# Kernel optimization log

Measured on AMD Instinct MI355X. Metric: run time of the kernel, lower is better.

The kernel has to match this reference:

```python
import jax, jax.numpy as jnp
import numpy as np
from jax import lax


def _conv2d(x, w, b):
    # Plain VALID conv, NCHW / OIHW, stride 1 (matches nn.Conv2d(kernel_size=3))
    y = lax.conv_general_dilated(x, w, (1, 1), 'VALID',
                                 dimension_numbers=('NCHW', 'OIHW', 'NCHW'))
    return y + b.reshape(1, -1, 1, 1)


def _deform_conv2d(x, w, b, offset, mask):
    # Faithful torchvision.ops.DeformConv2d: stride 1, pad 0, dilation 1, groups 1.
    # offset: [B, 2*K, Ho, Wo] with (dy, dx) interleaved per kernel tap.
    B, C, H, W = x.shape
    Cout, _, KH, KW = w.shape
    K = KH * KW
    Ho, Wo = H - KH + 1, W - KW + 1
    off = offset.reshape(B, K, 2, Ho, Wo)
    ky, kx = jnp.meshgrid(jnp.arange(KH), jnp.arange(KW), indexing='ij')  # [KH,KW]
    ky = ky.reshape(1, K, 1, 1).astype(off.dtype)
    kx = kx.reshape(1, K, 1, 1).astype(off.dtype)
    # sampling positions p = p0 + p_k + offset
    py = off[:, :, 0] + ky + jnp.arange(Ho, dtype=off.dtype).reshape(1, 1, Ho, 1)  # [B,K,Ho,Wo]
    px = off[:, :, 1] + kx + jnp.arange(Wo, dtype=off.dtype).reshape(1, 1, 1, Wo)
    y0 = jnp.floor(py)
    x0 = jnp.floor(px)
    fy = py - y0
    fx = px - x0
    y0i = y0.astype(jnp.int32)
    x0i = x0.astype(jnp.int32)
    x_flat = x.reshape(B, C, H * W)

    def corner(yi, xi, wgt):
        # zero-padding outside image: invalid taps contribute 0
        valid = (yi >= 0) & (yi < H) & (xi >= 0) & (xi < W)
        idx = jnp.clip(yi, 0, H - 1) * W + jnp.clip(xi, 0, W - 1)  # [B,K,Ho,Wo]
        vals = jax.vmap(lambda xf, i: jnp.take(xf, i, axis=-1))(x_flat, idx)  # [B,C,K,Ho,Wo]
        return vals * (wgt * valid)[:, None]

    acc = corner(y0i, x0i, (1 - fy) * (1 - fx))
    acc = acc + corner(y0i, x0i + 1, (1 - fy) * fx)
    acc = acc + corner(y0i + 1, x0i, fy * (1 - fx))
    acc = acc + corner(y0i + 1, x0i + 1, fy * fx)
    if mask is not None:
        acc = acc * mask.reshape(B, 1, K, Ho, Wo)
    out = jnp.einsum('bckhw,ock->bohw', acc, w.reshape(Cout, C, K))
    return out + b.reshape(1, -1, 1, 1)


def setup_inputs() -> dict:
    key = jax.random.key(0)
    ks = jax.random.split(key, 9)
    B, Cin, H, W = 16, 12, 256, 256
    s = 0.05  # small init so learned offsets stay a few pixels
    return {
        'x':  jax.random.normal(ks[0], (B, Cin, H, W), jnp.float32),
        'w0': jax.random.normal(ks[1], (18, Cin, 3, 3), jnp.float32) * s,
        'b0': jax.random.normal(ks[2], (18,), jnp.float32) * s,
        'w1': jax.random.normal(ks[3], (16, Cin, 3, 3), jnp.float32) * s,
        'b1': jax.random.normal(ks[4], (16,), jnp.float32) * s,
        'w2': jax.random.normal(ks[5], (9, Cin, 3, 3), jnp.float32) * s,
        'b2': jax.random.normal(ks[6], (9,), jnp.float32) * s,
        'w3': jax.random.normal(ks[7], (16, Cin, 3, 3), jnp.float32) * s,
        'b3': jax.random.normal(ks[8], (16,), jnp.float32) * s,
    }


def reference(x, w0, b0, w1, b1, w2, b2, w3, b3):
    offset = _conv2d(x, w0, b0)                       # [B,18,254,254]
    x1 = _deform_conv2d(x, w1, b1, offset, None)      # [B,16,254,254]
    mask = jax.nn.sigmoid(_conv2d(x, w2, b2))         # [B,9,254,254]
    x2 = _deform_conv2d(x, w3, b3, offset, mask)      # [B,16,254,254]
    return (x1, x2)
```

## Files before the change

kernel.cpp:

```cpp
#include <hip/hip_runtime.h>
#include <math.h>

#define BATCH 16
#define CIN   12
#define HH    256
#define WW    256
#define KK    9
#define HO    254
#define WO    254
#define PIX   (HO*WO)
#define COUT  16
#define CHW   (HH*WW)

__device__ __forceinline__ int iclamp(int v, int lo, int hi) {
    return v < lo ? lo : (v > hi ? hi : v);
}

__global__ __launch_bounds__(256, 4) void dcn_f32(
    const float* __restrict__ x,
    const float* __restrict__ w0, const float* __restrict__ b0,
    const float* __restrict__ w1, const float* __restrict__ b1,
    const float* __restrict__ w2, const float* __restrict__ b2,
    const float* __restrict__ w3, const float* __restrict__ b3,
    float* __restrict__ out)
{
    __shared__ float wc[KK*CIN*28];
    __shared__ float ew[KK*CIN*32];

    const int tid = threadIdx.y*16 + threadIdx.x;

    for (int i = tid; i < KK*CIN*28; i += 256) {
        int k = i / (CIN*28);
        int r = i % (CIN*28);
        int c = r / 28;
        int o = r % 28;
        float v = 0.f;
        if (o < 18)      v = w0[(o*CIN + c)*KK + k];
        else if (o < 27) v = w2[((o-18)*CIN + c)*KK + k];
        wc[i] = v;
    }
    for (int i = tid; i < KK*CIN*32; i += 256) {
        int kc = i >> 5;
        int j  = i & 31;
        int k  = kc / CIN;
        int c  = kc % CIN;
        ew[i] = (j < 16) ? w1[(j*CIN + c)*KK + k]
                         : w3[((j-16)*CIN + c)*KK + k];
    }
    __syncthreads();

    const int b  = blockIdx.z;
    const int ho = blockIdx.y*16 + threadIdx.y;
    const int wo = blockIdx.x*16 + threadIdx.x;
    if (ho >= HO || wo >= WO) return;

    const float* xb = x + (size_t)b*CIN*CHW;

    float off[28];
    #pragma unroll
    for (int o = 0; o < 18; ++o) off[o] = b0[o];
    #pragma unroll
    for (int o = 0; o < 9;  ++o) off[18+o] = b2[o];
    off[27] = 0.f;

    #pragma unroll
    for (int k = 0; k < 9; ++k) {
        const int ky = k / 3, kx = k % 3;
        const float* xt = xb + (size_t)(ho+ky)*WW + (wo+kx);
        float xv[CIN];
        #pragma unroll
        for (int c = 0; c < CIN; ++c) xv[c] = xt[(size_t)c*CHW];
        #pragma unroll
        for (int c = 0; c < CIN; ++c) {
            const float v = xv[c];
            const float4* wrow = (const float4*)&wc[(k*CIN + c)*28];
            #pragma unroll
            for (int q = 0; q < 7; ++q) {
                float4 w4 = wrow[q];
                off[4*q+0] += w4.x * v;
                off[4*q+1] += w4.y * v;
                off[4*q+2] += w4.z * v;
                off[4*q+3] += w4.w * v;
            }
        }
    }

    float m[9];
    #pragma unroll
    for (int j = 0; j < 9; ++j) m[j] = 1.f / (1.f + expf(-off[18+j]));

    float acc1[16], acc2[16];
    #pragma unroll
    for (int o = 0; o < 16; ++o) { acc1[o] = b1[o]; acc2[o] = b3[o]; }

    #pragma unroll
    for (int k = 0; k < 9; ++k) {
        const float py = off[2*k]   + (float)(k/3) + (float)ho;
        const float px = off[2*k+1] + (float)(k%3) + (float)wo;
        const float y0f = floorf(py), x0f = floorf(px);
        const float fy = py - y0f, fx = px - x0f;
        const int y0 = (int)y0f, x0i = (int)x0f;
        const int y1 = y0 + 1,  x1i = x0i + 1;

        float w00 = (1.f-fy)*(1.f-fx);
        float w01 = (1.f-fy)*fx;
        float w10 = fy*(1.f-fx);
        float w11 = fy*fx;

        const bool vy0 = (unsigned)y0  < HH;
        const bool vy1 = (unsigned)y1  < HH;
        const bool vx0 = (unsigned)x0i < WW;
        const bool vx1 = (unsigned)x1i < WW;
        if (!(vy0 && vx0)) w00 = 0.f;
        if (!(vy0 && vx1)) w01 = 0.f;
        if (!(vy1 && vx0)) w10 = 0.f;
        if (!(vy1 && vx1)) w11 = 0.f;

        const int cy0 = iclamp(y0, 0, HH-1);
        const int cy1 = iclamp(y1, 0, HH-1);
        const int cx0 = iclamp(x0i, 0, WW-1);
        const int cx1 = iclamp(x1i, 0, WW-1);
        const int i00 = cy0*WW + cx0;
        const int i01 = cy0*WW + cx1;
        const int i10 = cy1*WW + cx0;
        const int i11 = cy1*WW + cx1;

        const float mk = m[k];

        #pragma unroll
        for (int h = 0; h < 2; ++h) {
            float g00[6], g01[6], g10[6], g11[6];
            #pragma unroll
            for (int j = 0; j < 6; ++j) {
                const float* xc = xb + (size_t)(6*h + j)*CHW;
                g00[j] = xc[i00];
                g01[j] = xc[i01];
                g10[j] = xc[i10];
                g11[j] = xc[i11];
            }
            #pragma unroll
            for (int j = 0; j < 6; ++j) {
                const int c = 6*h + j;
                const float v  = w00*g00[j] + w01*g01[j] + w10*g10[j] + w11*g11[j];
                const float vm = v * mk;
                const float4* wr = (const float4*)&ew[(k*CIN + c)*32];
                #pragma unroll
                for (int q = 0; q < 4; ++q) {
                    float4 a  = wr[q];
                    float4 bb = wr[q+4];
                    acc1[4*q+0] += a.x  * v;
                    acc1[4*q+1] += a.y  * v;
                    acc1[4*q+2] += a.z  * v;
                    acc1[4*q+3] += a.w  * v;
                    acc2[4*q+0] += bb.x * vm;
                    acc2[4*q+1] += bb.y * vm;
                    acc2[4*q+2] += bb.z * vm;
                    acc2[4*q+3] += bb.w * vm;
                }
            }
        }
    }

    const size_t p = (size_t)ho*WO + wo;
    float* o1 = out + (size_t)b*COUT*PIX + p;
    float* o2 = o1 + (size_t)BATCH*COUT*PIX;
    #pragma unroll
    for (int o = 0; o < 16; ++o) {
        o1[(size_t)o*PIX] = acc1[o];
        o2[(size_t)o*PIX] = acc2[o];
    }
}

extern "C" void kernel_launch(void* const* d_in, const int* in_sizes, int n_in,
                              void* d_out, int out_size, void* d_ws, size_t ws_size,
                              hipStream_t stream) {
    const float* x  = (const float*)d_in[0];
    const float* w0 = (const float*)d_in[1];
    const float* b0 = (const float*)d_in[2];
    const float* w1 = (const float*)d_in[3];
    const float* b1 = (const float*)d_in[4];
    const float* w2 = (const float*)d_in[5];
    const float* b2 = (const float*)d_in[6];
    const float* w3 = (const float*)d_in[7];
    const float* b3 = (const float*)d_in[8];
    float* out = (float*)d_out;

    dim3 block(16, 16);
    dim3 grid((WO + 15)/16, (HO + 15)/16, BATCH);
    dcn_f32<<<grid, block, 0, stream>>>(x, w0, b0, w1, b1, w2, b2, w3, b3, out);
}
```

Before: 422.7 us.

## Rewrite deformable conv with split-fp16 MFMA GEMMs and per-row pixel tiles

Replaces the per-pixel FP32 kernel with one where each block handles 64 output pixels of a row. The offset and mask conv is split across four wavefronts by input channel and reduced through shared memory. The sampled values are then staged in shared memory as hi/lo fp16 pairs and contracted with the weights using 16x16x32 f16 MFMA in a three-product split that approximates fp32. The aim is to move the dense channel-mixing FLOPs onto matrix cores and spread gather work across waves. The cost is extra syncs, a lower occupancy bound, and a small precision change from the fp16 splitting.

```diff
diff --git a/kernel.cpp b/kernel.cpp
--- a/kernel.cpp
+++ b/kernel.cpp
@@ -1,22 +1,34 @@
 #include <hip/hip_runtime.h>
+#include <hip/hip_fp16.h>
 #include <math.h>
 
 #define BATCH 16
 #define CIN   12
 #define HH    256
 #define WW    256
-#define KK    9
 #define HO    254
 #define WO    254
 #define PIX   (HO*WO)
 #define COUT  16
 #define CHW   (HH*WW)
 
+typedef __attribute__((ext_vector_type(8))) _Float16 f16x8;
+typedef __attribute__((ext_vector_type(4))) float f32x4;
+
+__device__ __forceinline__ unsigned int f2h(float f) {
+    return (unsigned int)__half_as_ushort(__float2half(f));
+}
+__device__ __forceinline__ unsigned long long pk4h(float a, float b, float c, float d) {
+    unsigned int lo = f2h(a) | (f2h(b) << 16);
+    unsigned int hi = f2h(c) | (f2h(d) << 16);
+    return (unsigned long long)lo | ((unsigned long long)hi << 32);
+}
+__device__ __forceinline__ float hi_f(float v) { return (float)(_Float16)v; }
 __device__ __forceinline__ int iclamp(int v, int lo, int hi) {
     return v < lo ? lo : (v > hi ? hi : v);
 }
 
-__global__ __launch_bounds__(256, 4) void dcn_f32(
+__global__ __launch_bounds__(256, 2) void dcn_hl(
     const float* __restrict__ x,
     const float* __restrict__ w0, const float* __restrict__ b0,
     const float* __restrict__ w1, const float* __restrict__ b1,
@@ -24,150 +36,230 @@
     const float* __restrict__ w3, const float* __restrict__ b3,
     float* __restrict__ out)
 {
-    __shared__ float wc[KK*CIN*28];
-    __shared__ float ew[KK*CIN*32];
-
-    const int tid = threadIdx.y*16 + threadIdx.x;
-
-    for (int i = tid; i < KK*CIN*28; i += 256) {
-        int k = i / (CIN*28);
-        int r = i % (CIN*28);
-        int c = r / 28;
-        int o = r % 28;
-        float v = 0.f;
-        if (o < 18)      v = w0[(o*CIN + c)*KK + k];
-        else if (o < 27) v = w2[((o-18)*CIN + c)*KK + k];
-        wc[i] = v;
-    }
-    for (int i = tid; i < KK*CIN*32; i += 256) {
-        int kc = i >> 5;
-        int j  = i & 31;
-        int k  = kc / CIN;
-        int c  = kc % CIN;
-        ew[i] = (j < 16) ? w1[(j*CIN + c)*KK + k]
-                         : w3[((j-16)*CIN + c)*KK + k];
-    }
-    __syncthreads();
-
-    const int b  = blockIdx.z;
-    const int ho = blockIdx.y*16 + threadIdx.y;
-    const int wo = blockIdx.x*16 + threadIdx.x;
-    if (ho >= HO || wo >= WO) return;
-
-    const float* xb = x + (size_t)b*CIN*CHW;
-
-    float off[28];
+    __shared__ __align__(16) unsigned char AB[2*64*256];
+    __shared__ float off_s[64][28];
+
+    const int tid = threadIdx.x;
+    const int p   = tid & 63;
+    const int s   = __builtin_amdgcn_readfirstlane(tid >> 6);
+    const int l15 = p & 15;
+    const int l4  = p >> 4;
+
+    const int b   = blockIdx.z;
+    const int ho  = blockIdx.y;
+    const int wo0 = blockIdx.x * 64;
+    const int wo  = min(wo0 + p, WO - 1);
+    const float* xb = x + (size_t)b * (CIN*CHW);
+
+    unsigned char* Ahb = AB;
+    unsigned char* Alb = AB + 64*256;
+
+    {
+        float po[27];
+        #pragma unroll
+        for (int o = 0; o < 27; ++o) po[o] = 0.f;
+        #pragma unroll
+        for (int j = 0; j < 3; ++j) {
+            const int c = 3*s + j;
+            const float* xc = xb + (size_t)c*CHW + (size_t)ho*WW + wo;
+            #pragma unroll
+            for (int k = 0; k < 9; ++k) {
+                const float v = xc[(k/3)*WW + (k%3)];
+                #pragma unroll
+                for (int o = 0; o < 18; ++o) po[o]    += v * w0[(o*CIN + c)*9 + k];
+                #pragma unroll
+                for (int o = 0; o < 9;  ++o) po[18+o] += v * w2[(o*CIN + c)*9 + k];
+            }
+        }
+        float* part = (float*)AB;
+        #pragma unroll
+        for (int o = 0; o < 27; ++o) part[(s*64 + p)*28 + o] = po[o];
+    }
+    __syncthreads();
+
+    {
+        const float* part = (const float*)AB;
+        #pragma unroll
+        for (int j = 0; j < 7; ++j) {
+            const int o = s*7 + j;
+            if (o < 27) {
+                float v = part[(0*64+p)*28 + o] + part[(1*64+p)*28 + o]
+                        + part[(2*64+p)*28 + o] + part[(3*64+p)*28 + o];
+                if (o < 18) v += b0[o];
+                else        v = 1.f / (1.f + expf(-(v + b2[o-18])));
+                off_s[p][o] = v;
+            }
+        }
+    }
+    __syncthreads();
+
+    float vm[7][4];
+    {
+        #pragma unroll
+        for (int i = 0; i < 7; ++i) {
+            const int u = s*7 + i;
+            if (u < 27) {
+                const int k = u/3, jq = u - k*3;
+                const float dy = off_s[p][2*k], dx = off_s[p][2*k+1];
+                const float mk = off_s[p][18 + k];
+                const float py = dy + (float)(k/3) + (float)ho;
+                const float px = dx + (float)(k%3) + (float)wo;
+                const float y0f = floorf(py), x0f = floorf(px);
+                const float fy = py - y0f, fx = px - x0f;
+                const int y0 = (int)y0f, x0i = (int)x0f;
+                const int y1 = y0 + 1,  x1i = x0i + 1;
+                float w00 = (1.f-fy)*(1.f-fx);
+                float w01 = (1.f-fy)*fx;
+                float w10 = fy*(1.f-fx);
+                float w11 = fy*fx;
+                const bool vy0 = (unsigned)y0  < HH, vy1 = (unsigned)y1  < HH;
+                const bool vx0 = (unsigned)x0i < WW, vx1 = (unsigned)x1i < WW;
+                if (!(vy0 && vx0)) w00 = 0.f;
+                if (!(vy0 && vx1)) w01 = 0.f;
+                if (!(vy1 && vx0)) w10 = 0.f;
+                if (!(vy1 && vx1)) w11 = 0.f;
+                const int cy0 = iclamp(y0, 0, HH-1),  cy1 = iclamp(y1, 0, HH-1);
+                const int cx0 = iclamp(x0i, 0, WW-1), cx1 = iclamp(x1i, 0, WW-1);
+                const int i00 = cy0*WW + cx0, i01 = cy0*WW + cx1;
+                const int i10 = cy1*WW + cx0, i11 = cy1*WW + cx1;
+
+                float vv[4];
+                #pragma unroll
+                for (int c = 0; c < 4; ++c) {
+                    const float* xc = xb + (size_t)(4*jq + c)*CHW;
+                    vv[c] = w00*xc[i00] + w01*xc[i01] + w10*xc[i10] + w11*xc[i11];
+                    vm[i][c] = vv[c] * mk;
+                }
+                const int boff = k*24 + 8*jq;
+                *(unsigned long long*)(Ahb + p*256 + boff) =
+                    pk4h(vv[0], vv[1], vv[2], vv[3]);
+                *(unsigned long long*)(Alb + p*256 + boff) =
+                    pk4h((vv[0]-hi_f(vv[0]))*512.f, (vv[1]-hi_f(vv[1]))*512.f,
+                         (vv[2]-hi_f(vv[2]))*512.f, (vv[3]-hi_f(vv[3]))*512.f);
+            }
+        }
+        if (s < 3) {
+            *(unsigned long long*)(Ahb + p*256 + 216 + 8*s) = 0ull;
+            *(unsigned long long*)(Alb + p*256 + 216 + 8*s) = 0ull;
+        } else {
+            *(unsigned long long*)(Ahb + p*256 + 240) = 0ull;
+            *(unsigned long long*)(Alb + p*256 + 240) = 0ull;
+            *(unsigned long long*)(Ahb + p*256 + 248) = 0ull;
+            *(unsigned long long*)(Alb + p*256 + 248) = 0ull;
+        }
+    }
+
+    f16x8 beh[4], bel[4];
     #pragma unroll
-    for (int o = 0; o < 18; ++o) off[o] = b0[o];
+    for (int kk = 0; kk < 4; ++kk) {
+        f16x8 th, tl;
+        #pragma unroll
+        for (int ii = 0; ii < 8; ++ii) {
+            const int K = kk*32 + (l4 << 3) + ii;
+            float v = 0.f;
+            if (K < 108) {
+                const int tap = K/12, c = K%12;
+                v = w1[(l15*CIN + c)*9 + tap];
+            }
+            th[ii] = (_Float16)v;
+            tl[ii] = (_Float16)((v - hi_f(v)) * 512.f);
+        }
+        beh[kk] = th; bel[kk] = tl;
+    }
+    __syncthreads();
+
+    {
+        f32x4 aH = {0.f,0.f,0.f,0.f}, aL = {0.f,0.f,0.f,0.f};
+        const int rowA = s*16 + l15;
+        #pragma unroll
+        for (int kk = 0; kk < 4; ++kk) {
+            f16x8 ah = *(const f16x8*)(Ahb + rowA*256 + kk*64 + (l4 << 4));
+            f16x8 al = *(const f16x8*)(Alb + rowA*256 + kk*64 + (l4 << 4));
+            aH = __builtin_amdgcn_mfma_f32_16x16x32_f16(ah, beh[kk], aH, 0, 0, 0);
+            aL = __builtin_amdgcn_mfma_f32_16x16x32_f16(ah, bel[kk], aL, 0, 0, 0);
+            aL = __builtin_amdgcn_mfma_f32_16x16x32_f16(al, beh[kk], aL, 0, 0, 0);
+        }
+        const float bb = b1[l15];
+        const int wob = wo0 + s*16 + (l4 << 2);
+        float* dst = out + (size_t)(b*COUT + l15)*PIX + (size_t)ho*WO + wob;
+        float r[4];
+        #pragma unroll
+        for (int e = 0; e < 4; ++e) r[e] = aH[e] + aL[e]*(1.f/512.f) + bb;
+        if (wob + 4 <= WO) {
+            float2 r01; r01.x = r[0]; r01.y = r[1];
+            float2 r23; r23.x = r[2]; r23.y = r[3];
+            *(float2*)(dst)     = r01;
+            *(float2*)(dst + 2) = r23;
+        } else {
+            #pragma unroll
+            for (int e = 0; e < 4; ++e)
+                if (wob + e < WO) dst[e] = r[e];
+        }
+    }
+    __syncthreads();
+
+    {
+        #pragma unroll
+        for (int i = 0; i < 7; ++i) {
+            const int u = s*7 + i;
+            if (u < 27) {
+                const int k = u/3, jq = u - k*3;
+                const int boff = k*24 + 8*jq;
+                *(unsigned long long*)(Ahb + p*256 + boff) =
+                    pk4h(vm[i][0], vm[i][1], vm[i][2], vm[i][3]);
+                *(unsigned long long*)(Alb + p*256 + boff) =
+                    pk4h((vm[i][0]-hi_f(vm[i][0]))*512.f, (vm[i][1]-hi_f(vm[i][1]))*512.f,
+                         (vm[i][2]-hi_f(vm[i][2]))*512.f, (vm[i][3]-hi_f(vm[i][3]))*512.f);
+            }
+        }
+    }
+
     #pragma unroll
-    for (int o = 0; o < 9;  ++o) off[18+o] = b2[o];
-    off[27] = 0.f;
-
-    #pragma unroll
-    for (int k = 0; k < 9; ++k) {
-        const int ky = k / 3, kx = k % 3;
-        const float* xt = xb + (size_t)(ho+ky)*WW + (wo+kx);
-        float xv[CIN];
-        #pragma unroll
-        for (int c = 0; c < CIN; ++c) xv[c] = xt[(size_t)c*CHW];
-        #pragma unroll
-        for (int c = 0; c < CIN; ++c) {
-            const float v = xv[c];
-            const float4* wrow = (const float4*)&wc[(k*CIN + c)*28];
+    for (int kk = 0; kk < 4; ++kk) {
+        f16x8 th, tl;
+        #pragma unroll
+        for (int ii = 0; ii < 8; ++ii) {
+            const int K = kk*32 + (l4 << 3) + ii;
+            float v = 0.f;
+            if (K < 108) {
+                const int tap = K/12, c = K%12;
+                v = w3[(l15*CIN + c)*9 + tap];
+            }
+            th[ii] = (_Float16)v;
+            tl[ii] = (_Float16)((v - hi_f(v)) * 512.f);
+        }
+        beh[kk] = th; bel[kk] = tl;
+    }
+    __syncthreads();
+
+    {
+        f32x4 aH = {0.f,0.f,0.f,0.f}, aL = {0.f,0.f,0.f,0.f};
+        const int rowA = s*16 + l15;
+        #pragma unroll
+        for (int kk = 0; kk < 4; ++kk) {
+            f16x8 ah = *(const f16x8*)(Ahb + rowA*256 + kk*64 + (l4 << 4));
+            f16x8 al = *(const f16x8*)(Alb + rowA*256 + kk*64 + (l4 << 4));
+            aH = __builtin_amdgcn_mfma_f32_16x16x32_f16(ah, beh[kk], aH, 0, 0, 0);
+            aL = __builtin_amdgcn_mfma_f32_16x16x32_f16(ah, bel[kk], aL, 0, 0, 0);
+            aL = __builtin_amdgcn_mfma_f32_16x16x32_f16(al, beh[kk], aL, 0, 0, 0);
+        }
+        const float bb = b3[l15];
+        const int wob = wo0 + s*16 + (l4 << 2);
+        float* dst = out + (size_t)(BATCH*COUT)*PIX
+                         + (size_t)(b*COUT + l15)*PIX + (size_t)ho*WO + wob;
+        float r[4];
+        #pragma unroll
+        for (int e = 0; e < 4; ++e) r[e] = aH[e] + aL[e]*(1.f/512.f) + bb;
+        if (wob + 4 <= WO) {
+            float2 r01; r01.x = r[0]; r01.y = r[1];
+            float2 r23; r23.x = r[2]; r23.y = r[3];
+            *(float2*)(dst)     = r01;
+            *(float2*)(dst + 2) = r23;
+        } else {
             #pragma unroll
-            for (int q = 0; q < 7; ++q) {
-                float4 w4 = wrow[q];
-                off[4*q+0] += w4.x * v;
-                off[4*q+1] += w4.y * v;
-                off[4*q+2] += w4.z * v;
-                off[4*q+3] += w4.w * v;
-            }
-        }
-    }
-
-    float m[9];
-    #pragma unroll
-    for (int j = 0; j < 9; ++j) m[j] = 1.f / (1.f + expf(-off[18+j]));
-
-    float acc1[16], acc2[16];
-    #pragma unroll
-    for (int o = 0; o < 16; ++o) { acc1[o] = b1[o]; acc2[o] = b3[o]; }
-
-    #pragma unroll
-    for (int k = 0; k < 9; ++k) {
-        const float py = off[2*k]   + (float)(k/3) + (float)ho;
-        const float px = off[2*k+1] + (float)(k%3) + (float)wo;
-        const float y0f = floorf(py), x0f = floorf(px);
-        const float fy = py - y0f, fx = px - x0f;
-        const int y0 = (int)y0f, x0i = (int)x0f;
-        const int y1 = y0 + 1,  x1i = x0i + 1;
-
-        float w00 = (1.f-fy)*(1.f-fx);
-        float w01 = (1.f-fy)*fx;
-        float w10 = fy*(1.f-fx);
-        float w11 = fy*fx;
-
-        const bool vy0 = (unsigned)y0  < HH;
-        const bool vy1 = (unsigned)y1  < HH;
-        const bool vx0 = (unsigned)x0i < WW;
-        const bool vx1 = (unsigned)x1i < WW;
-        if (!(vy0 && vx0)) w00 = 0.f;
-        if (!(vy0 && vx1)) w01 = 0.f;
-        if (!(vy1 && vx0)) w10 = 0.f;
-        if (!(vy1 && vx1)) w11 = 0.f;
-
-        const int cy0 = iclamp(y0, 0, HH-1);
-        const int cy1 = iclamp(y1, 0, HH-1);
-        const int cx0 = iclamp(x0i, 0, WW-1);
-        const int cx1 = iclamp(x1i, 0, WW-1);
-        const int i00 = cy0*WW + cx0;
-        const int i01 = cy0*WW + cx1;
-        const int i10 = cy1*WW + cx0;
-        const int i11 = cy1*WW + cx1;
-
-        const float mk = m[k];
-
-        #pragma unroll
-        for (int h = 0; h < 2; ++h) {
-            float g00[6], g01[6], g10[6], g11[6];
-            #pragma unroll
-            for (int j = 0; j < 6; ++j) {
-                const float* xc = xb + (size_t)(6*h + j)*CHW;
-                g00[j] = xc[i00];
-                g01[j] = xc[i01];
-                g10[j] = xc[i10];
-                g11[j] = xc[i11];
-            }
-            #pragma unroll
-            for (int j = 0; j < 6; ++j) {
-                const int c = 6*h + j;
-                const float v  = w00*g00[j] + w01*g01[j] + w10*g10[j] + w11*g11[j];
-                const float vm = v * mk;
-                const float4* wr = (const float4*)&ew[(k*CIN + c)*32];
-                #pragma unroll
-                for (int q = 0; q < 4; ++q) {
-                    float4 a  = wr[q];
-                    float4 bb = wr[q+4];
-                    acc1[4*q+0] += a.x  * v;
-                    acc1[4*q+1] += a.y  * v;
-                    acc1[4*q+2] += a.z  * v;
-                    acc1[4*q+3] += a.w  * v;
-                    acc2[4*q+0] += bb.x * vm;
-                    acc2[4*q+1] += bb.y * vm;
-                    acc2[4*q+2] += bb.z * vm;
-                    acc2[4*q+3] += bb.w * vm;
-                }
-            }
-        }
-    }
-
-    const size_t p = (size_t)ho*WO + wo;
-    float* o1 = out + (size_t)b*COUT*PIX + p;
-    float* o2 = o1 + (size_t)BATCH*COUT*PIX;
-    #pragma unroll
-    for (int o = 0; o < 16; ++o) {
-        o1[(size_t)o*PIX] = acc1[o];
-        o2[(size_t)o*PIX] = acc2[o];
+            for (int e = 0; e < 4; ++e)
+                if (wob + e < WO) dst[e] = r[e];
+        }
     }
 }
 
@@ -185,7 +277,7 @@
     const float* b3 = (const float*)d_in[8];
     float* out = (float*)d_out;
 
-    dim3 block(16, 16);
-    dim3 grid((WO + 15)/16, (HO + 15)/16, BATCH);
-    dcn_f32<<<grid, block, 0, stream>>>(x, w0, b0, w1, b1, w2, b2, w3, b3, out);
-}
+    dim3 block(256);
+    dim3 grid(4, HO, BATCH);
+    dcn_hl<<<grid, block, 0, stream>>>(x, w0, b0, w1, b1, w2, b2, w3, b3, out);
+}
```

After: 581.2 us. 1.38x slower.
